# Kernel optimization log

Hardware: AMD Instinct MI355X
Metric: run time of the kernel (lower is better)

Reference implementation:

```python
import jax, jax.numpy as jnp
import numpy as np

KS = 5  # kernel_size


def _extract_patches(x, ks):
    # x: [B, C, H, W] -> [B, C, Ho, Wo, ks*ks] (VALID windows)
    B, C, H, W = x.shape
    Ho, Wo = H - ks + 1, W - ks + 1
    taps = [x[:, :, u:u + Ho, v:v + Wo] for u in range(ks) for v in range(ks)]
    return jnp.stack(taps, axis=-1)


def setup_inputs() -> dict:
    key = jax.random.key(0)
    k1, k2, k3 = jax.random.split(key, 3)
    B, C, H, W = 8, 3, 128, 128
    O, ks = 8, KS
    stdv = 1.0 / np.sqrt(C * ks * ks)
    x = jax.random.normal(k1, (B, C, H, W), dtype=jnp.float32)
    K_hit = jax.random.uniform(k2, (O, C, ks, ks), dtype=jnp.float32,
                               minval=-stdv, maxval=stdv)
    K_miss = jax.random.uniform(k3, (O, C, ks, ks), dtype=jnp.float32,
                                minval=-stdv, maxval=stdv)
    return {"x": x, "K_hit": K_hit, "K_miss": K_miss}


def reference(x, K_hit, K_miss):
    # Fmap[b, k*C+c, y, x] = min_{u,v}(patch - K_hit[k,c]) - max_{u,v}(patch - K_miss[k,c])
    O, C, ks, _ = K_hit.shape
    patches = _extract_patches(x, ks)                    # [B, C, Ho, Wo, ks*ks]
    B, _, Ho, Wo, P = patches.shape
    p = patches[:, None]                                 # [B, 1, C, Ho, Wo, P]
    kh = K_hit.reshape(O, C, P)[None, :, :, None, None, :]
    km = K_miss.reshape(O, C, P)[None, :, :, None, None, :]
    hit = jnp.min(p - kh, axis=-1)                       # [B, O, C, Ho, Wo]
    miss = jnp.max(p - km, axis=-1)                      # [B, O, C, Ho, Wo]
    fmap = hit - miss
    return fmap.reshape(B, O * C, Ho, Wo)
```

## Files before the change

kernel.cpp:

```cpp
#include <hip/hip_runtime.h>

#define B_    8
#define C_    3
#define O_    8
#define H_    128
#define W_    128
#define KS_   5
#define HO_   (H_ - KS_ + 1)
#define WO_   (W_ - KS_ + 1)
#define NPIX  (HO_ * WO_)
#define NTAP  (KS_ * KS_)
#define PX    2
#define NG    (WO_ / PX)
#define NPIXG (HO_ * NG)
#define BLK   256

__global__ __launch_bounds__(BLK)
void mnn_kernel(const float* __restrict__ x,
                const float* __restrict__ Kh,
                const float* __restrict__ Km,
                float* __restrict__ out)
{
    const int bc = blockIdx.y;
    const int b  = bc / C_;
    const int c  = bc % C_;

    const int p = blockIdx.x * BLK + threadIdx.x;
    if (p >= NPIXG) return;
    const int ho  = p / NG;
    const int wo0 = (p % NG) * PX;

    float w[KS_][KS_ + PX - 1];
    const float* xrow = x + ((b * C_ + c) * H_ + ho) * W_ + wo0;
#pragma unroll
    for (int u = 0; u < KS_; ++u) {
#pragma unroll
        for (int v2 = 0; v2 < (KS_ + PX - 1 + 1) / 2; ++v2) {
            const float2 t = *reinterpret_cast<const float2*>(xrow + u * W_ + v2 * 2);
            w[u][v2 * 2 + 0] = t.x;
            w[u][v2 * 2 + 1] = t.y;
        }
    }

    const float* khc = Kh + c * NTAP;
    const float* kmc = Km + c * NTAP;

    const size_t obase = ((size_t)b * (O_ * C_) + c) * (size_t)NPIX
                       + (size_t)ho * WO_ + wo0;

#pragma unroll
    for (int o = 0; o < O_; ++o) {
        float hit0  =  INFINITY, hit1  =  INFINITY;
        float miss0 = -INFINITY, miss1 = -INFINITY;
#pragma unroll
        for (int u = 0; u < KS_; ++u) {
#pragma unroll
            for (int v = 0; v < KS_; ++v) {
                const int t = u * KS_ + v;
                const float kh = khc[o * (C_ * NTAP) + t];
                const float km = kmc[o * (C_ * NTAP) + t];
                hit0  = fminf(hit0,  w[u][v]     - kh);
                hit1  = fminf(hit1,  w[u][v + 1] - kh);
                miss0 = fmaxf(miss0, w[u][v]     - km);
                miss1 = fmaxf(miss1, w[u][v + 1] - km);
            }
        }
        float2 r;
        r.x = hit0 - miss0;
        r.y = hit1 - miss1;
        *reinterpret_cast<float2*>(out + obase + (size_t)o * (C_ * NPIX)) = r;
    }
}

extern "C" void kernel_launch(void* const* d_in, const int* in_sizes, int n_in,
                              void* d_out, int out_size, void* d_ws, size_t ws_size,
                              hipStream_t stream)
{
    const float* x  = (const float*)d_in[0];
    const float* Kh = (const float*)d_in[1];
    const float* Km = (const float*)d_in[2];
    float* out = (float*)d_out;

    dim3 grid((NPIXG + BLK - 1) / BLK, B_ * C_);
    dim3 block(BLK);
    mnn_kernel<<<grid, block, 0, stream>>>(x, Kh, Km, out);
}
```

Baseline: 65.75 us.

## Compute four output pixels per thread with float4 loads and min3-style chains

Each thread now produces four adjacent output pixels instead of two, so every loaded input window row feeds more outputs. The input window is fetched with two float4 loads per row. The tap loop is restructured into pairs of chained fminf/fmaxf, which the compiler can fuse into 3-input min/max instructions. Outputs are written with a float4 nontemporal store to avoid polluting the cache. The trade-off is higher register pressure per thread and half as many threads in flight.

```diff
diff --git a/kernel.cpp b/kernel.cpp
--- a/kernel.cpp
+++ b/kernel.cpp
@@ -10,10 +10,12 @@
 #define WO_   (W_ - KS_ + 1)
 #define NPIX  (HO_ * WO_)
 #define NTAP  (KS_ * KS_)
-#define PX    2
+#define PX    4
 #define NG    (WO_ / PX)
 #define NPIXG (HO_ * NG)
 #define BLK   256
+
+typedef float floatx4 __attribute__((ext_vector_type(4)));
 
 __global__ __launch_bounds__(BLK)
 void mnn_kernel(const float* __restrict__ x,
@@ -35,10 +37,12 @@
 #pragma unroll
     for (int u = 0; u < KS_; ++u) {
 #pragma unroll
-        for (int v2 = 0; v2 < (KS_ + PX - 1 + 1) / 2; ++v2) {
-            const float2 t = *reinterpret_cast<const float2*>(xrow + u * W_ + v2 * 2);
-            w[u][v2 * 2 + 0] = t.x;
-            w[u][v2 * 2 + 1] = t.y;
+        for (int v4 = 0; v4 < 2; ++v4) {
+            const floatx4 t = *reinterpret_cast<const floatx4*>(xrow + u * W_ + v4 * 4);
+            w[u][v4 * 4 + 0] = t.x;
+            w[u][v4 * 4 + 1] = t.y;
+            w[u][v4 * 4 + 2] = t.z;
+            w[u][v4 * 4 + 3] = t.w;
         }
     }
 
@@ -50,25 +54,38 @@
 
 #pragma unroll
     for (int o = 0; o < O_; ++o) {
-        float hit0  =  INFINITY, hit1  =  INFINITY;
-        float miss0 = -INFINITY, miss1 = -INFINITY;
+        const float* kh = khc + o * (C_ * NTAP);
+        const float* km = kmc + o * (C_ * NTAP);
+
+        float hit[PX], miss[PX];
+        {
+            const float kh0 = kh[0], km0 = km[0];
 #pragma unroll
-        for (int u = 0; u < KS_; ++u) {
-#pragma unroll
-            for (int v = 0; v < KS_; ++v) {
-                const int t = u * KS_ + v;
-                const float kh = khc[o * (C_ * NTAP) + t];
-                const float km = kmc[o * (C_ * NTAP) + t];
-                hit0  = fminf(hit0,  w[u][v]     - kh);
-                hit1  = fminf(hit1,  w[u][v + 1] - kh);
-                miss0 = fmaxf(miss0, w[u][v]     - km);
-                miss1 = fmaxf(miss1, w[u][v + 1] - km);
+            for (int q = 0; q < PX; ++q) {
+                hit[q]  = w[0][q] - kh0;
+                miss[q] = w[0][q] - km0;
             }
         }
-        float2 r;
-        r.x = hit0 - miss0;
-        r.y = hit1 - miss1;
-        *reinterpret_cast<float2*>(out + obase + (size_t)o * (C_ * NPIX)) = r;
+#pragma unroll
+        for (int t = 1; t < NTAP; t += 2) {
+            const int u0 = t / KS_,       v0 = t % KS_;
+            const int u1 = (t + 1) / KS_, v1 = (t + 1) % KS_;
+            const float kh0 = kh[t], kh1 = kh[t + 1];
+            const float km0 = km[t], km1 = km[t + 1];
+#pragma unroll
+            for (int q = 0; q < PX; ++q) {
+                hit[q]  = fminf(fminf(hit[q],  w[u0][v0 + q] - kh0), w[u1][v1 + q] - kh1);
+                miss[q] = fmaxf(fmaxf(miss[q], w[u0][v0 + q] - km0), w[u1][v1 + q] - km1);
+            }
+        }
+
+        floatx4 r;
+        r.x = hit[0] - miss[0];
+        r.y = hit[1] - miss[1];
+        r.z = hit[2] - miss[2];
+        r.w = hit[3] - miss[3];
+        __builtin_nontemporal_store(r,
+            reinterpret_cast<floatx4*>(out + obase + (size_t)o * (C_ * NPIX)));
     }
 }
 
```

After: 69.46 us. +5.6%, slower.
